# Optimization experiments

Hardware: AMD Instinct MI355X
Metric: run time of the kernel (lower is better)

The kernel has to match this reference:

```python
import jax, jax.numpy as jnp
import numpy as np

B, S, D, H, FF = 4, 1024, 1024, 16, 4096
HD = D // H
SCALE = float(np.sqrt(HD))
LAMBDA_MIN = 0.5
LAMBDA_MAX = 0.5
EPS = 1e-5


def _layernorm(x, g, b):
    mu = jnp.mean(x, axis=-1, keepdims=True)
    var = jnp.mean(jnp.square(x - mu), axis=-1, keepdims=True)
    return (x - mu) * jax.lax.rsqrt(var + EPS) * g + b


def _qbnn_layer(h, W, bW, J, lam_base, g, be):
    # s_prev = tanh(h); h_tilde = h W + b; delta_j = (sum_i s_prev_i J_ij) * tanh(h_tilde)_j
    s_prev = jnp.tanh(h)
    h_tilde = h @ W + bW
    s_raw = jnp.tanh(h_tilde)
    delta = (s_prev @ J) * s_raw
    lam_n = jax.nn.sigmoid(lam_base)
    dynamic_factor = 0.5  # eval mode, call_count=0 -> 0.5+0.5*sin(0)
    lam_eff = LAMBDA_MIN + (LAMBDA_MAX - LAMBDA_MIN) * (lam_n * 0.7 + dynamic_factor * 0.3)
    h_hat = h_tilde + lam_eff * delta
    return jax.nn.gelu(_layernorm(h_hat, g, be), approximate=False)


def setup_inputs() -> dict:
    key = jax.random.key(0)
    ks = jax.random.split(key, 24)
    f32 = jnp.float32
    lin = lambda k, i, o: jax.random.normal(k, (i, o), f32) / np.sqrt(i)
    inp = {
        'x': jax.random.normal(ks[0], (B, S, D), f32),
        # attention projections (stored as [in, out]; y = x @ W + b)
        'wq': lin(ks[1], D, D), 'bq': jnp.zeros((D,), f32),
        'wk': lin(ks[2], D, D), 'bk': jnp.zeros((D,), f32),
        'wv': lin(ks[3], D, D), 'bv': jnp.zeros((D,), f32),
        'wo': lin(ks[4], D, D), 'bo': jnp.zeros((D,), f32),
        'J_attn': jax.random.normal(ks[5], (H, HD, HD), f32) * 0.02,
        'lambda_attn': jnp.asarray(0.5, f32),
        'g_attn': jnp.ones((D,), f32), 'b_attn': jnp.zeros((D,), f32),
        # ffn layer 1 (D -> FF)
        'W1': lin(ks[6], D, FF), 'b1': jnp.zeros((FF,), f32),
        'J1': jax.random.normal(ks[7], (D, FF), f32) * 0.02,
        'lam1': jnp.asarray(0.5, f32),
        'g1': jnp.ones((FF,), f32), 'be1': jnp.zeros((FF,), f32),
        # ffn layer 2 (FF -> D)
        'W2': lin(ks[8], FF, D), 'b2': jnp.zeros((D,), f32),
        'J2': jax.random.normal(ks[9], (FF, D), f32) * 0.02,
        'lam2': jnp.asarray(0.5, f32),
        'g2': jnp.ones((D,), f32), 'be2': jnp.zeros((D,), f32),
        # ffn pre-norm
        'g_ffn': jnp.ones((D,), f32), 'b_ffn': jnp.zeros((D,), f32),
    }
    return inp


def reference(x, wq, bq, wk, bk, wv, bv, wo, bo, J_attn, lambda_attn, g_attn, b_attn,
              W1, b1, J1, lam1, g1, be1, W2, b2, J2, lam2, g2, be2, g_ffn, b_ffn):
    # --- attention (pre-norm) ---
    xn = _layernorm(x, g_attn, b_attn)
    split = lambda t: t.reshape(B, S, H, HD).transpose(0, 2, 1, 3)  # bshd -> bhsd
    Q = split(xn @ wq + bq)
    K = split(xn @ wk + bk)
    V = split(xn @ wv + bv)
    scores = jnp.einsum('bhid,bhjd->bhij', Q, K) / SCALE
    tQJ = jnp.einsum('bhid,hde->bhie', jnp.tanh(Q), J_attn)
    delta = jnp.einsum('bhie,bhje->bhij', tQJ, jnp.tanh(K))
    probs = jax.nn.softmax(scores + lambda_attn * delta, axis=-1)
    attn = jnp.einsum('bhij,bhjd->bhid', probs, V)
    attn = attn.transpose(0, 2, 1, 3).reshape(B, S, D) @ wo + bo
    x = x + attn
    # --- QBNN FFN (pre-norm) ---
    h = _layernorm(x, g_ffn, b_ffn)
    h = _qbnn_layer(h, W1, b1, J1, lam1, g1, be1)
    h = _qbnn_layer(h, W2, b2, J2, lam2, g2, be2)
    return x + h
```

## Files before the change

kernel.cpp:

```cpp
#include <hip/hip_runtime.h>
#include <cmath>

typedef unsigned short u16;
typedef unsigned int   u32;
typedef short bhalf8 __attribute__((ext_vector_type(8)));
typedef float fx4    __attribute__((ext_vector_type(4)));

#define B_   4
#define S_   1024
#define D_   1024
#define H_   16
#define HD_  64
#define FF_  4096
#define NTOK (B_*S_)
#define QKVW 3072

__device__ __forceinline__ float b2f(u16 u) {
    u32 x = ((u32)u) << 16;
    return __uint_as_float(x);
}
__device__ __forceinline__ u16 f2b(float f) {
    u32 u = __float_as_uint(f);
    u32 r = (u + 0x7fffu + ((u >> 16) & 1u)) >> 16;
    return (u16)r;
}

#define GLDS16(g, l) __builtin_amdgcn_global_load_lds( \
    (const __attribute__((address_space(1))) void*)(g), \
    (__attribute__((address_space(3))) void*)(l), 16, 0, 0)

__device__ __forceinline__ void tile_swz(int gx, int gy, int& bx, int& by) {
    int bid = blockIdx.x;
    int nwg = gx * gy;
    if (((nwg | gy) & 7) == 0) {
        int chunk = nwg >> 3;
        int wg = (bid & 7) * chunk + (bid >> 3);
        int tps = gx << 3;
        int sup = wg / tps, rem = wg % tps;
        bx = rem >> 3;
        by = (sup << 3) + (rem & 7);
    } else {
        bx = bid % gx; by = bid / gx;
    }
}

__global__ __launch_bounds__(256) void cvt_t_k(const float* __restrict__ w0, const float* __restrict__ w1,
                                               const float* __restrict__ w2, const float* __restrict__ w3,
                                               const float* __restrict__ W1p, const float* __restrict__ J1p,
                                               const float* __restrict__ W2p, const float* __restrict__ J2p,
                                               u16* __restrict__ dst) {
    __shared__ u16 L[64][65];
    int bid = blockIdx.x, tid = threadIdx.x;
    const float* src; size_t dbase; int Kd, Nd, tk, tn;
    if (bid < 1024)      { int m = bid >> 8, t = bid & 255;
                           src = m == 0 ? w0 : m == 1 ? w1 : m == 2 ? w2 : w3;
                           dbase = (size_t)m << 20; Kd = 1024; Nd = 1024; tk = t >> 4; tn = t & 15; }
    else if (bid < 2048) { int t = bid - 1024; src = W1p; dbase = (size_t)4  << 20; Kd = 1024; Nd = 4096; tk = t >> 6; tn = t & 63; }
    else if (bid < 3072) { int t = bid - 2048; src = J1p; dbase = (size_t)8  << 20; Kd = 1024; Nd = 4096; tk = t >> 6; tn = t & 63; }
    else if (bid < 4096) { int t = bid - 3072; src = W2p; dbase = (size_t)12 << 20; Kd = 4096; Nd = 1024; tk = t >> 4; tn = t & 15; }
    else                 { int t = bid - 4096; src = J2p; dbase = (size_t)16 << 20; Kd = 4096; Nd = 1024; tk = t >> 4; tn = t & 15; }
    int k0 = tk * 64, n0 = tn * 64;
    int r = tid >> 2, c4 = (tid & 3) * 16;
    #pragma unroll
    for (int p = 0; p < 4; ++p) {
        float4 v = *(const float4*)&src[(size_t)(k0 + r) * Nd + n0 + c4 + p * 4];
        L[r][c4 + p * 4 + 0] = f2b(v.x);
        L[r][c4 + p * 4 + 1] = f2b(v.y);
        L[r][c4 + p * 4 + 2] = f2b(v.z);
        L[r][c4 + p * 4 + 3] = f2b(v.w);
    }
    __syncthreads();
    u16 o[16];
    #pragma unroll
    for (int j = 0; j < 16; ++j) o[j] = L[c4 + j][r];
    *(uint4*)&dst[dbase + (size_t)(n0 + r) * Kd + k0 + c4]     = *(uint4*)&o[0];
    *(uint4*)&dst[dbase + (size_t)(n0 + r) * Kd + k0 + c4 + 8] = *(uint4*)&o[8];
}

__global__ __launch_bounds__(256) void tanh_k(const u16* __restrict__ in, u16* __restrict__ outb) {
    size_t idx = ((size_t)blockIdx.x * 256 + threadIdx.x) * 8;
    uint4 v = *(const uint4*)&in[idx];
    const u16* p = (const u16*)&v;
    u16 o[8];
    #pragma unroll
    for (int j = 0; j < 8; ++j) o[j] = f2b(tanhf(b2f(p[j])));
    *(uint4*)&outb[idx] = *(uint4*)o;
}

template <int EPI, bool SEG>
__global__ __launch_bounds__(256, 2) void gemm128(const u16* __restrict__ A,
                                                  const u16* __restrict__ Bt,
                                                  const float* __restrict__ bA,
                                                  const float* __restrict__ bB,
                                                  const float* __restrict__ bC,
                                                  const float* __restrict__ resid,
                                                  void* __restrict__ Cout,
                                                  int M, int N, int K) {
    __shared__ u16 As[128 * 32];
    __shared__ u16 Bs[128 * 32];
    const int tid = threadIdx.x;
    const int w = tid >> 6, ln = tid & 63;
    const int q = ln >> 4, mr = ln & 15;
    int bx, by;
    tile_swz(N >> 7, M >> 7, bx, by);
    const int m0 = by * 128, n0 = bx * 128;
    const int wm = (w >> 1) * 64, wn = (w & 1) * 64;
    const int sr = w * 16 + (ln >> 2);
    const int sc = ((ln & 3) ^ ((ln >> 2) & 3)) * 8;
    const int qx = (q ^ (mr & 3)) * 8;

    fx4 acc[4][4];
    #pragma unroll
    for (int i = 0; i < 4; ++i)
        #pragma unroll
        for (int j = 0; j < 4; ++j) acc[i][j] = (fx4){0.f, 0.f, 0.f, 0.f};

    const u16* Ab0 = A  + (size_t)(m0 + sr) * K + sc;
    const u16* Ab1 = A  + (size_t)(m0 + sr + 64) * K + sc;
    const u16* Bb0 = Bt + (size_t)(n0 + sr) * K + sc;
    const u16* Bb1 = Bt + (size_t)(n0 + sr + 64) * K + sc;

    for (int k0 = 0; k0 < K; k0 += 32) {
        __syncthreads();
        GLDS16(Ab0 + k0, &As[w * 512]);
        GLDS16(Ab1 + k0, &As[(w + 4) * 512]);
        GLDS16(Bb0 + k0, &Bs[w * 512]);
        GLDS16(Bb1 + k0, &Bs[(w + 4) * 512]);
        __syncthreads();

        bhalf8 af[4], bf[4];
        #pragma unroll
        for (int i = 0; i < 4; ++i) af[i] = *(const bhalf8*)&As[(wm + i * 16 + mr) * 32 + qx];
        #pragma unroll
        for (int j = 0; j < 4; ++j) bf[j] = *(const bhalf8*)&Bs[(wn + j * 16 + mr) * 32 + qx];
        #pragma unroll
        for (int i = 0; i < 4; ++i)
            #pragma unroll
            for (int j = 0; j < 4; ++j)
                acc[i][j] = __builtin_amdgcn_mfma_f32_16x16x32_bf16(af[i], bf[j], acc[i][j], 0, 0, 0);
    }

    #pragma unroll
    for (int j = 0; j < 4; ++j) {
        int col = n0 + wn + j * 16 + mr;
        float bs;
        if (SEG) {
            const float* bp = col < 1024 ? bA : (col < 2048 ? bB : bC);
            bs = bp[col & 1023];
        } else {
            bs = bA ? bA[col] : 0.f;
        }
        #pragma unroll
        for (int i = 0; i < 4; ++i) {
            #pragma unroll
            for (int r = 0; r < 4; ++r) {
                int row    = m0 + wm + i * 16 + q * 4 + r;
                size_t idx = (size_t)row * N + col;
                float v    = acc[i][j][r] + bs;
                if (EPI == 0) {
                    ((u16*)Cout)[idx] = f2b(v);
                } else if (EPI == 1) {
                    ((float*)Cout)[idx] = v + resid[idx];
                } else {
                    float ht = b2f(((u16*)Cout)[idx]);
                    ((u16*)Cout)[idx] = f2b(ht + 0.5f * v * tanhf(ht));
                }
            }
        }
    }
}

__global__ __launch_bounds__(256, 2) void dgemm128(const u16* __restrict__ A,
                                                   const u16* __restrict__ At,
                                                   const u16* __restrict__ WT,
                                                   const u16* __restrict__ JT,
                                                   const float* __restrict__ bias,
                                                   u16* __restrict__ Cout,
                                                   int M, int N, int K) {
    __shared__ u16 As[128 * 32];
    __shared__ u16 Ts[128 * 32];
    __shared__ u16 Ws[128 * 32];
    __shared__ u16 Js[128 * 32];
    const int tid = threadIdx.x;
    const int w = tid >> 6, ln = tid & 63;
    const int q = ln >> 4, mr = ln & 15;
    int bx, by;
    tile_swz(N >> 7, M >> 7, bx, by);
    const int m0 = by * 128, n0 = bx * 128;
    const int wm = (w >> 1) * 64, wn = (w & 1) * 64;
    const int sr = w * 16 + (ln >> 2);
    const int sc = ((ln & 3) ^ ((ln >> 2) & 3)) * 8;
    const int qx = (q ^ (mr & 3)) * 8;

    fx4 aw[4][4], aj[4][4];
    #pragma unroll
    for (int i = 0; i < 4; ++i)
        #pragma unroll
        for (int j = 0; j < 4; ++j) {
            aw[i][j] = (fx4){0.f, 0.f, 0.f, 0.f};
            aj[i][j] = (fx4){0.f, 0.f, 0.f, 0.f};
        }

    const u16* Ab0 = A  + (size_t)(m0 + sr) * K + sc;
    const u16* Ab1 = A  + (size_t)(m0 + sr + 64) * K + sc;
    const u16* Tb0 = At + (size_t)(m0 + sr) * K + sc;
    const u16* Tb1 = At + (size_t)(m0 + sr + 64) * K + sc;
    const u16* Wb0 = WT + (size_t)(n0 + sr) * K + sc;
    const u16* Wb1 = WT + (size_t)(n0 + sr + 64) * K + sc;
    const u16* Jb0 = JT + (size_t)(n0 + sr) * K + sc;
    const u16* Jb1 = JT + (size_t)(n0 + sr + 64) * K + sc;

    for (int k0 = 0; k0 < K; k0 += 32) {
        __syncthreads();
        GLDS16(Ab0 + k0, &As[w * 512]);
        GLDS16(Ab1 + k0, &As[(w + 4) * 512]);
        GLDS16(Tb0 + k0, &Ts[w * 512]);
        GLDS16(Tb1 + k0, &Ts[(w + 4) * 512]);
        GLDS16(Wb0 + k0, &Ws[w * 512]);
        GLDS16(Wb1 + k0, &Ws[(w + 4) * 512]);
        GLDS16(Jb0 + k0, &Js[w * 512]);
        GLDS16(Jb1 + k0, &Js[(w + 4) * 512]);
        __syncthreads();

        bhalf8 af[4], tf[4];
        #pragma unroll
        for (int i = 0; i < 4; ++i) {
            af[i] = *(const bhalf8*)&As[(wm + i * 16 + mr) * 32 + qx];
            tf[i] = *(const bhalf8*)&Ts[(wm + i * 16 + mr) * 32 + qx];
        }
        #pragma unroll
        for (int j = 0; j < 4; ++j) {
            bhalf8 wf = *(const bhalf8*)&Ws[(wn + j * 16 + mr) * 32 + qx];
            bhalf8 jf = *(const bhalf8*)&Js[(wn + j * 16 + mr) * 32 + qx];
            #pragma unroll
            for (int i = 0; i < 4; ++i) {
                aw[i][j] = __builtin_amdgcn_mfma_f32_16x16x32_bf16(af[i], wf, aw[i][j], 0, 0, 0);
                aj[i][j] = __builtin_amdgcn_mfma_f32_16x16x32_bf16(tf[i], jf, aj[i][j], 0, 0, 0);
            }
        }
    }

    #pragma unroll
    for (int j = 0; j < 4; ++j) {
        int col = n0 + wn + j * 16 + mr;
        float bs = bias[col];
        #pragma unroll
        for (int i = 0; i < 4; ++i) {
            #pragma unroll
            for (int r = 0; r < 4; ++r) {
                int row    = m0 + wm + i * 16 + q * 4 + r;
                size_t idx = (size_t)row * N + col;
                float ht   = aw[i][j][r] + bs;
                Cout[idx]  = f2b(ht + 0.5f * aj[i][j][r] * tanhf(ht));
            }
        }
    }
}

__global__ __launch_bounds__(256) void ln_k(const float* __restrict__ xin,
                                            const float* __restrict__ g,
                                            const float* __restrict__ bb,
                                            u16* __restrict__ out, int W) {
    __shared__ float red[8], red2[8], stats[2];
    int row = blockIdx.x, tid = threadIdx.x;
    float s = 0.f, ss = 0.f;
    for (int c = tid; c < W; c += 256) {
        float v = xin[(size_t)row * W + c];
        s += v; ss += v * v;
    }
    #pragma unroll
    for (int off = 32; off; off >>= 1) { s += __shfl_xor(s, off); ss += __shfl_xor(ss, off); }
    int wave = tid >> 6, lane = tid & 63;
    if (lane == 0) { red[wave] = s; red2[wave] = ss; }
    __syncthreads();
    if (tid == 0) {
        float S = 0.f, SS = 0.f;
        for (int w2 = 0; w2 < 4; ++w2) { S += red[w2]; SS += red2[w2]; }
        float mu = S / W;
        stats[0] = mu;
        stats[1] = rsqrtf(SS / W - mu * mu + 1e-5f);
    }
    __syncthreads();
    float mu = stats[0], rs = stats[1];
    for (int c = tid; c < W; c += 256)
        out[(size_t)row * W + c] = f2b((xin[(size_t)row * W + c] - mu) * rs * g[c] + bb[c]);
}

template <bool RES, bool OUT_F32>
__global__ __launch_bounds__(256) void lngelu_k(const u16* __restrict__ u,
                                                const float* __restrict__ g,
                                                const float* __restrict__ be,
                                                const float* __restrict__ resid,
                                                void* __restrict__ out, int W) {
    __shared__ float ub[4096];
    __shared__ float red[8], red2[8], stats[2];
    int row = blockIdx.x, tid = threadIdx.x;
    float s = 0.f, ss = 0.f;
    for (int c = tid; c < W; c += 256) {
        float v = b2f(u[(size_t)row * W + c]);
        ub[c] = v; s += v; ss += v * v;
    }
    #pragma unroll
    for (int off = 32; off; off >>= 1) { s += __shfl_xor(s, off); ss += __shfl_xor(ss, off); }
    int wave = tid >> 6, lane = tid & 63;
    if (lane == 0) { red[wave] = s; red2[wave] = ss; }
    __syncthreads();
    if (tid == 0) {
        float S = 0.f, SS = 0.f;
        for (int w2 = 0; w2 < 4; ++w2) { S += red[w2]; SS += red2[w2]; }
        float mu = S / W;
        stats[0] = mu;
        stats[1] = rsqrtf(SS / W - mu * mu + 1e-5f);
    }
    __syncthreads();
    float mu = stats[0], rs = stats[1];
    for (int c = tid; c < W; c += 256) {
        float v = (ub[c] - mu) * rs * g[c] + be[c];
        float y = 0.5f * v * (1.f + erff(v * 0.70710678118654752f));
        if (RES) y += resid[(size_t)row * W + c];
        if (OUT_F32) ((float*)out)[(size_t)row * W + c] = y;
        else         ((u16*)out)[(size_t)row * W + c] = f2b(y);
    }
}

__global__ __launch_bounds__(256) void aug_q_k(const u16* __restrict__ QKV,
                                               const float* __restrict__ J,
                                               const float* __restrict__ lamp,
                                               u16* __restrict__ QA) {
    __shared__ float Jl[64][68];
    __shared__ float Tq[64][65];
    int blk = blockIdx.x;
    int bh = blk >> 4, st = blk & 15;
    int b = bh >> 4, h = bh & 15;
    int s0 = st * 64;
    int tid = threadIdx.x;
    float lam = lamp[0];

    for (int i = tid; i < 4096; i += 256)
        Jl[i >> 6][i & 63] = J[h * 4096 + i];
    for (int i = tid; i < 4096; i += 256) {
        int r = i >> 6, c = i & 63;
        float v  = b2f(QKV[(size_t)(b * S_ + s0 + r) * QKVW + h * 64 + c]);
        Tq[r][c] = tanhf(v);
        QA[((size_t)(bh * S_ + s0 + r)) * 128 + c] = f2b(v * 0.125f);
    }
    __syncthreads();

    int r = tid >> 2, c0 = (tid & 3) * 16;
    float acc[16];
    #pragma unroll
    for (int j = 0; j < 16; ++j) acc[j] = 0.f;
    for (int k = 0; k < 64; ++k) {
        float a = Tq[r][k];
        #pragma unroll
        for (int j4 = 0; j4 < 4; ++j4) {
            float4 jv = *(const float4*)&Jl[k][c0 + j4 * 4];
            acc[j4 * 4 + 0] += a * jv.x;
            acc[j4 * 4 + 1] += a * jv.y;
            acc[j4 * 4 + 2] += a * jv.z;
            acc[j4 * 4 + 3] += a * jv.w;
        }
    }
    size_t orow = ((size_t)(bh * S_ + s0 + r)) * 128 + 64 + c0;
    #pragma unroll
    for (int j = 0; j < 16; ++j) QA[orow + j] = f2b(lam * acc[j]);
}

__global__ __launch_bounds__(256) void aug_k_k(const u16* __restrict__ QKV,
                                               u16* __restrict__ KA) {
    int idx = blockIdx.x * 256 + threadIdx.x;
    int d = idx & (D_ - 1);
    int bs = idx >> 10;
    int h = d >> 6, hd = d & 63;
    int b = bs >> 10, si = bs & (S_ - 1);
    u16 v      = QKV[(size_t)bs * QKVW + 1024 + d];
    size_t row = (size_t)((b * H_ + h) * S_ + si);
    KA[row * 128 + hd]      = v;
    KA[row * 128 + 64 + hd] = f2b(tanhf(b2f(v)));
}

#define QS_STRIDE 136
#define PS_STRIDE 72
__global__ __launch_bounds__(256) void attn_k(const u16* __restrict__ QA,
                                              const u16* __restrict__ KA,
                                              const u16* __restrict__ QKV,
                                              u16* __restrict__ out) {
    __shared__ u16 Qs[64 * QS_STRIDE];
    __shared__ u16 Ks[64 * QS_STRIDE];
    __shared__ u16 Vt[64 * PS_STRIDE];
    __shared__ u16 Ps[4 * 16 * PS_STRIDE];

    const int tid  = threadIdx.x;
    const int w    = tid >> 6, lane = tid & 63;
    const int q    = lane >> 4, mr = lane & 15;
    const int bh   = blockIdx.x >> 4;
    const int qt   = blockIdx.x & 15;
    const int b    = bh >> 4, h = bh & 15;

    #pragma unroll
    for (int p = 0; p < 4; ++p) {
        int idx = p * 2048 + tid * 8;
        int row = idx >> 7, col = idx & 127;
        uint4 v4 = *(const uint4*)&QA[((size_t)(bh * S_ + qt * 64 + row)) * 128 + col];
        *(uint4*)&Qs[row * QS_STRIDE + col] = v4;
    }

    fx4 zero = {0.f, 0.f, 0.f, 0.f};
    fx4 O[4] = {zero, zero, zero, zero};
    float m[4]  = {-3e38f, -3e38f, -3e38f, -3e38f};
    float l[4]  = {0.f, 0.f, 0.f, 0.f};

    for (int kt = 0; kt < 16; ++kt) {
        #pragma unroll
        for (int p = 0; p < 4; ++p) {
            int idx = p * 2048 + tid * 8;
            int row = idx >> 7, col = idx & 127;
            uint4 v4 = *(const uint4*)&KA[((size_t)(bh * S_ + kt * 64 + row)) * 128 + col];
            *(uint4*)&Ks[row * QS_STRIDE + col] = v4;
        }
        #pragma unroll
        for (int p = 0; p < 2; ++p) {
            int idx = p * 2048 + tid * 8;
            int key = idx >> 6, d0 = idx & 63;
            uint4 v4 = *(const uint4*)&QKV[((size_t)(b * S_ + kt * 64 + key)) * QKVW + 2048 + h * 64 + d0];
            const u16* vp = (const u16*)&v4;
            #pragma unroll
            for (int j = 0; j < 8; ++j) Vt[(d0 + j) * PS_STRIDE + key] = vp[j];
        }
        __syncthreads();

        fx4 St[4] = {zero, zero, zero, zero};
        bhalf8 afr[4];
        #pragma unroll
        for (int ks = 0; ks < 4; ++ks)
            afr[ks] = *(const bhalf8*)&Qs[(w * 16 + mr) * QS_STRIDE + ks * 32 + q * 8];
        __builtin_amdgcn_s_setprio(1);
        #pragma unroll
        for (int nt = 0; nt < 4; ++nt) {
            #pragma unroll
            for (int ks = 0; ks < 4; ++ks) {
                bhalf8 bf = *(const bhalf8*)&Ks[(nt * 16 + mr) * QS_STRIDE + ks * 32 + q * 8];
                St[nt] = __builtin_amdgcn_mfma_f32_16x16x32_bf16(afr[ks], bf, St[nt], 0, 0, 0);
            }
        }
        __builtin_amdgcn_s_setprio(0);

        float alpha[4];
        #pragma unroll
        for (int r = 0; r < 4; ++r) {
            float mx = fmaxf(fmaxf(St[0][r], St[1][r]), fmaxf(St[2][r], St[3][r]));
            #pragma unroll
            for (int off = 8; off; off >>= 1) mx = fmaxf(mx, __shfl_xor(mx, off));
            float nm = fmaxf(m[r], mx);
            alpha[r] = __expf(m[r] - nm);
            m[r] = nm;
            float ps = 0.f;
            #pragma unroll
            for (int nt = 0; nt < 4; ++nt) {
                float p = __expf(St[nt][r] - nm);
                St[nt][r] = p;
                ps += p;
            }
            #pragma unroll
            for (int off = 8; off; off >>= 1) ps += __shfl_xor(ps, off);
            l[r] = l[r] * alpha[r] + ps;
        }
        #pragma unroll
        for (int nt = 0; nt < 4; ++nt) {
            #pragma unroll
            for (int r = 0; r < 4; ++r) {
                Ps[(w * 16 + q * 4 + r) * PS_STRIDE + nt * 16 + mr] = f2b(St[nt][r]);
                O[nt][r] *= alpha[r];
            }
        }

        __builtin_amdgcn_s_setprio(1);
        #pragma unroll
        for (int ks = 0; ks < 2; ++ks) {
            bhalf8 pa = *(const bhalf8*)&Ps[(w * 16 + mr) * PS_STRIDE + ks * 32 + q * 8];
            #pragma unroll
            for (int nt = 0; nt < 4; ++nt) {
                bhalf8 bf = *(const bhalf8*)&Vt[(nt * 16 + mr) * PS_STRIDE + ks * 32 + q * 8];
                O[nt] = __builtin_amdgcn_mfma_f32_16x16x32_bf16(pa, bf, O[nt], 0, 0, 0);
            }
        }
        __builtin_amdgcn_s_setprio(0);
        __syncthreads();
    }

    #pragma unroll
    for (int nt = 0; nt < 4; ++nt) {
        int d = nt * 16 + mr;
        #pragma unroll
        for (int r = 0; r < 4; ++r) {
            int row = qt * 64 + w * 16 + q * 4 + r;
            out[((size_t)(b * S_ + row)) * D_ + h * 64 + d] = f2b(O[nt][r] / l[r]);
        }
    }
}

extern "C" void kernel_launch(void* const* d_in, const int* in_sizes, int n_in,
                              void* d_out, int out_size, void* d_ws, size_t ws_size,
                              hipStream_t stream) {
    const float* x      = (const float*)d_in[0];
    const float* wq     = (const float*)d_in[1];
    const float* bq     = (const float*)d_in[2];
    const float* wk     = (const float*)d_in[3];
    const float* bk     = (const float*)d_in[4];
    const float* wv     = (const float*)d_in[5];
    const float* bv     = (const float*)d_in[6];
    const float* wo     = (const float*)d_in[7];
    const float* bo     = (const float*)d_in[8];
    const float* Jattn  = (const float*)d_in[9];
    const float* lamA   = (const float*)d_in[10];
    const float* g_attn = (const float*)d_in[11];
    const float* b_attn = (const float*)d_in[12];
    const float* W1     = (const float*)d_in[13];
    const float* b1     = (const float*)d_in[14];
    const float* J1     = (const float*)d_in[15];
    const float* g1     = (const float*)d_in[17];
    const float* be1    = (const float*)d_in[18];
    const float* W2     = (const float*)d_in[19];
    const float* b2     = (const float*)d_in[20];
    const float* J2     = (const float*)d_in[21];
    const float* g2     = (const float*)d_in[23];
    const float* be2    = (const float*)d_in[24];
    const float* g_ffn  = (const float*)d_in[25];
    const float* b_ffn  = (const float*)d_in[26];
    float* out = (float*)d_out;
    (void)in_sizes; (void)n_in; (void)out_size;

    char* wsp = (char*)d_ws;
    const size_t MB = 1u << 20;
    u16* WB = (u16*)(wsp);
    const u16* qkvT = WB;
    const u16* woT  = WB + ((size_t)3 << 20);
    const u16* W1T  = WB + ((size_t)4 << 20);
    const u16* J1T  = WB + ((size_t)8 << 20);
    const u16* W2T  = WB + ((size_t)12 << 20);
    const u16* J2T  = WB + ((size_t)16 << 20);
    u16*   XN   = (u16*)(wsp + 40 * MB);
    u16*   AT   = (u16*)(wsp + 40 * MB);
    u16*   Ht1  = (u16*)(wsp + 40 * MB);
    u16*   U2   = (u16*)(wsp + 40 * MB);
    u16*   QKVb = (u16*)(wsp + 48 * MB);
    u16*   Hb   = (u16*)(wsp + 48 * MB);
    float* X2   = (float*)(wsp + 56 * MB);
    u16*   QA   = (u16*)(wsp + 72 * MB);
    u16*   KA   = (u16*)(wsp + 88 * MB);
    u16*   U1   = (u16*)(wsp + 72 * MB);
    u16*   Ht2  = (u16*)(wsp + 104 * MB);
    const bool dual2 = ws_size >= 136 * MB;

    dim3 blk(256);
    cvt_t_k<<<5120, blk, 0, stream>>>(wq, wk, wv, wo, W1, J1, W2, J2, WB);
    ln_k<<<NTOK, blk, 0, stream>>>(x, g_attn, b_attn, XN, D_);
    gemm128<0, true><<<(QKVW / 128) * (NTOK / 128), blk, 0, stream>>>(XN, qkvT, bq, bk, bv, nullptr, QKVb, NTOK, QKVW, D_);
    aug_q_k<<<B_ * H_ * (S_ / 64), blk, 0, stream>>>(QKVb, Jattn, lamA, QA);
    aug_k_k<<<(NTOK * D_) / 256, blk, 0, stream>>>(QKVb, KA);
    attn_k<<<B_ * H_ * (S_ / 64), blk, 0, stream>>>(QA, KA, QKVb, AT);
    gemm128<1, false><<<(D_ / 128) * (NTOK / 128), blk, 0, stream>>>(AT, woT, bo, nullptr, nullptr, x, X2, NTOK, D_, D_);
    ln_k<<<NTOK, blk, 0, stream>>>(X2, g_ffn, b_ffn, Hb, D_);
    tanh_k<<<(NTOK * D_) / 2048, blk, 0, stream>>>(Hb, Ht1);
    dgemm128<<<(FF_ / 128) * (NTOK / 128), blk, 0, stream>>>(Hb, Ht1, W1T, J1T, b1, U1, NTOK, FF_, D_);
    lngelu_k<false, false><<<NTOK, blk, 0, stream>>>(U1, g1, be1, nullptr, U1, FF_);
    if (dual2) {
        tanh_k<<<(NTOK * FF_) / 2048, blk, 0, stream>>>(U1, Ht2);
        dgemm128<<<(D_ / 128) * (NTOK / 128), blk, 0, stream>>>(U1, Ht2, W2T, J2T, b2, U2, NTOK, D_, FF_);
    } else {
        gemm128<0, false><<<(D_ / 128) * (NTOK / 128), blk, 0, stream>>>(U1, W2T, b2, nullptr, nullptr, nullptr, U2, NTOK, D_, FF_);
        tanh_k<<<(NTOK * FF_) / 2048, blk, 0, stream>>>(U1, U1);
        gemm128<2, false><<<(D_ / 128) * (NTOK / 128), blk, 0, stream>>>(U1, J2T, nullptr, nullptr, nullptr, nullptr, U2, NTOK, D_, FF_);
    }
    lngelu_k<true, true><<<NTOK, blk, 0, stream>>>(U2, g2, be2, X2, out, D_);
}
```

Measured before the change: 705.1 us.

## Double-buffer dual GEMM LDS tiles and adjust LDS swizzle pattern

The dual-accumulator GEMM now uses two LDS buffers, issuing global-to-LDS loads for the next K tile before computing the current one, with explicit vmcnt waits and raw barriers instead of two __syncthreads per iteration. It also raises wave priority around the MFMA block. Both GEMM kernels switch the XOR swizzle so a different lane/row bit selects the chunk, meant to reduce LDS bank conflicts. Double buffering doubles LDS use (64KB per block), which may limit occupancy below the launch-bounds target of 2 blocks per CU.

```diff
diff --git a/kernel.cpp b/kernel.cpp
--- a/kernel.cpp
+++ b/kernel.cpp
@@ -106,8 +106,8 @@
     const int m0 = by * 128, n0 = bx * 128;
     const int wm = (w >> 1) * 64, wn = (w & 1) * 64;
     const int sr = w * 16 + (ln >> 2);
-    const int sc = ((ln & 3) ^ ((ln >> 2) & 3)) * 8;
-    const int qx = (q ^ (mr & 3)) * 8;
+    const int sc = ((ln & 3) ^ ((ln >> 3) & 3)) * 8;
+    const int qx = (q ^ ((mr >> 1) & 3)) * 8;
 
     fx4 acc[4][4];
     #pragma unroll
@@ -177,10 +177,10 @@
                                                    const float* __restrict__ bias,
                                                    u16* __restrict__ Cout,
                                                    int M, int N, int K) {
-    __shared__ u16 As[128 * 32];
-    __shared__ u16 Ts[128 * 32];
-    __shared__ u16 Ws[128 * 32];
-    __shared__ u16 Js[128 * 32];
+    __shared__ u16 As[2][128 * 32];
+    __shared__ u16 Ts[2][128 * 32];
+    __shared__ u16 Ws[2][128 * 32];
+    __shared__ u16 Js[2][128 * 32];
     const int tid = threadIdx.x;
     const int w = tid >> 6, ln = tid & 63;
     const int q = ln >> 4, mr = ln & 15;
@@ -189,8 +189,8 @@
     const int m0 = by * 128, n0 = bx * 128;
     const int wm = (w >> 1) * 64, wn = (w & 1) * 64;
     const int sr = w * 16 + (ln >> 2);
-    const int sc = ((ln & 3) ^ ((ln >> 2) & 3)) * 8;
-    const int qx = (q ^ (mr & 3)) * 8;
+    const int sc = ((ln & 3) ^ ((ln >> 3) & 3)) * 8;
+    const int qx = (q ^ ((mr >> 1) & 3)) * 8;
 
     fx4 aw[4][4], aj[4][4];
     #pragma unroll
@@ -210,35 +210,52 @@
     const u16* Jb0 = JT + (size_t)(n0 + sr) * K + sc;
     const u16* Jb1 = JT + (size_t)(n0 + sr + 64) * K + sc;
 
-    for (int k0 = 0; k0 < K; k0 += 32) {
-        __syncthreads();
-        GLDS16(Ab0 + k0, &As[w * 512]);
-        GLDS16(Ab1 + k0, &As[(w + 4) * 512]);
-        GLDS16(Tb0 + k0, &Ts[w * 512]);
-        GLDS16(Tb1 + k0, &Ts[(w + 4) * 512]);
-        GLDS16(Wb0 + k0, &Ws[w * 512]);
-        GLDS16(Wb1 + k0, &Ws[(w + 4) * 512]);
-        GLDS16(Jb0 + k0, &Js[w * 512]);
-        GLDS16(Jb1 + k0, &Js[(w + 4) * 512]);
-        __syncthreads();
+#define DG_STAGE(pp, kk) do { \
+        GLDS16(Ab0 + (kk), &As[pp][w * 512]); \
+        GLDS16(Ab1 + (kk), &As[pp][(w + 4) * 512]); \
+        GLDS16(Tb0 + (kk), &Ts[pp][w * 512]); \
+        GLDS16(Tb1 + (kk), &Ts[pp][(w + 4) * 512]); \
+        GLDS16(Wb0 + (kk), &Ws[pp][w * 512]); \
+        GLDS16(Wb1 + (kk), &Ws[pp][(w + 4) * 512]); \
+        GLDS16(Jb0 + (kk), &Js[pp][w * 512]); \
+        GLDS16(Jb1 + (kk), &Js[pp][(w + 4) * 512]); \
+    } while (0)
+
+    const int NT = K >> 5;
+    DG_STAGE(0, 0);
+    int p = 0;
+    for (int t = 0; t < NT; ++t) {
+        if (t + 1 < NT) {
+            DG_STAGE(p ^ 1, (t + 1) << 5);
+            asm volatile("s_waitcnt vmcnt(8)" ::: "memory");
+        } else {
+            asm volatile("s_waitcnt vmcnt(0)" ::: "memory");
+        }
+        __builtin_amdgcn_s_barrier();
 
         bhalf8 af[4], tf[4];
         #pragma unroll
         for (int i = 0; i < 4; ++i) {
-            af[i] = *(const bhalf8*)&As[(wm + i * 16 + mr) * 32 + qx];
-            tf[i] = *(const bhalf8*)&Ts[(wm + i * 16 + mr) * 32 + qx];
-        }
+            af[i] = *(const bhalf8*)&As[p][(wm + i * 16 + mr) * 32 + qx];
+            tf[i] = *(const bhalf8*)&Ts[p][(wm + i * 16 + mr) * 32 + qx];
+        }
+        __builtin_amdgcn_s_setprio(1);
         #pragma unroll
         for (int j = 0; j < 4; ++j) {
-            bhalf8 wf = *(const bhalf8*)&Ws[(wn + j * 16 + mr) * 32 + qx];
-            bhalf8 jf = *(const bhalf8*)&Js[(wn + j * 16 + mr) * 32 + qx];
+            bhalf8 wf = *(const bhalf8*)&Ws[p][(wn + j * 16 + mr) * 32 + qx];
+            bhalf8 jf = *(const bhalf8*)&Js[p][(wn + j * 16 + mr) * 32 + qx];
             #pragma unroll
             for (int i = 0; i < 4; ++i) {
                 aw[i][j] = __builtin_amdgcn_mfma_f32_16x16x32_bf16(af[i], wf, aw[i][j], 0, 0, 0);
                 aj[i][j] = __builtin_amdgcn_mfma_f32_16x16x32_bf16(tf[i], jf, aj[i][j], 0, 0, 0);
             }
         }
-    }
+        __builtin_amdgcn_s_setprio(0);
+        asm volatile("s_waitcnt lgkmcnt(0)" ::: "memory");
+        __builtin_amdgcn_s_barrier();
+        p ^= 1;
+    }
+#undef DG_STAGE
 
     #pragma unroll
     for (int j = 0; j < 4; ++j) {
```

After: 694.9 us. No clear change (-1.5%).
